# Performance work log

Hardware: AMD Instinct MI355X
Metric: run time of the kernel (lower is better)

The kernel has to match this reference:

```python
import jax, jax.numpy as jnp
import numpy as np

EPS = 1e-05


def layer_norm(x, a, b):
    m = jnp.mean(x, axis=-1, keepdims=True)
    v = jnp.var(x, axis=-1, keepdims=True)
    return a * (x - m) / jnp.sqrt(v + EPS) + b


def setup_inputs() -> dict:
    key = jax.random.key(0)
    ks = jax.random.split(key, 16)
    b, n, d, h = 1, 384, 128, 128
    s = 1.0 / np.sqrt(d)
    inp = {
        "x": jax.random.normal(ks[0], (b, n, n, d), dtype=jnp.float32),
        "norm_a": jnp.ones((d,), jnp.float32),
        "norm_b": jnp.zeros((d,), jnp.float32),
        "Wl": jax.random.normal(ks[1], (d, h), jnp.float32) * s,
        "bl": jnp.zeros((h,), jnp.float32),
        "Wr": jax.random.normal(ks[2], (d, h), jnp.float32) * s,
        "br": jnp.zeros((h,), jnp.float32),
        "Wlg": jax.random.normal(ks[3], (d, h), jnp.float32) * s,
        "blg": jnp.ones((h,), jnp.float32),
        "Wrg": jax.random.normal(ks[4], (d, h), jnp.float32) * s,
        "brg": jnp.ones((h,), jnp.float32),
        "Wog": jax.random.normal(ks[5], (d, h), jnp.float32) * s,
        "bog": jnp.ones((h,), jnp.float32),
        "on_a": jnp.ones((h,), jnp.float32),
        "on_b": jnp.zeros((h,), jnp.float32),
        "Wo": jax.random.normal(ks[6], (h, d), jnp.float32) * s,
        "bo": jnp.zeros((d,), jnp.float32),
    }
    return inp


def reference(x, norm_a, norm_b, Wl, bl, Wr, br, Wlg, blg, Wrg, brg, Wog, bog, on_a, on_b, Wo, bo):
    n = x.shape[1]
    xn = layer_norm(x, norm_a, norm_b)
    left = (xn @ Wl + bl) * jax.nn.sigmoid(xn @ Wlg + blg)
    right = (xn @ Wr + br) * jax.nn.sigmoid(xn @ Wrg + brg)
    out_gate = jax.nn.sigmoid(xn @ Wog + bog)
    # ingoing mix: out[b,i,j,d] = sum_k left[b,k,j,d] * right[b,k,i,d], in fp32
    out = jnp.einsum('bkjd,bkid->bijd', left.astype(jnp.float32), right.astype(jnp.float32)) / n
    out = out.astype(x.dtype)
    out = layer_norm(out, on_a, on_b) * out_gate
    return out @ Wo + bo
```

## Files before the change

### kernel.cpp

```cpp
#include <hip/hip_runtime.h>
#include <hip/hip_bf16.h>

#define NN 384
#define DD 128
#define MM (NN*NN)

typedef __attribute__((ext_vector_type(8))) short short8;
typedef __attribute__((ext_vector_type(4))) float f32x4;

__device__ __forceinline__ unsigned short f2bf(float f){
  unsigned u = __float_as_uint(f);
  u += 0x7fffu + ((u >> 16) & 1u);
  return (unsigned short)(u >> 16);
}
__device__ __forceinline__ float bf2f(unsigned short u){
  return __uint_as_float(((unsigned)u) << 16);
}
__device__ __forceinline__ float sigm(float x){
  return 1.0f / (1.0f + __expf(-x));
}
__device__ __forceinline__ unsigned cvtpk(float lo, float hi){
  unsigned r;
  asm("v_cvt_pk_bf16_f32 %0, %1, %2" : "=v"(r) : "v"(lo), "v"(hi));
  return r;
}
__device__ __forceinline__ f32x4 mfma16(short8 a, short8 b, f32x4 c){
  return __builtin_amdgcn_mfma_f32_16x16x32_bf16(a, b, c, 0, 0, 0);
}
__device__ __forceinline__ void gll16(const void* g, void* l){
  __builtin_amdgcn_global_load_lds(
      (const __attribute__((address_space(1))) unsigned int*)g,
      (__attribute__((address_space(3))) unsigned int*)l, 16, 0, 0);
}

__global__ void k_prep(const float* __restrict__ Wl, const float* __restrict__ Wlg,
                       const float* __restrict__ Wr, const float* __restrict__ Wrg,
                       const float* __restrict__ Wog, const float* __restrict__ Wo,
                       unsigned short* __restrict__ Wcat, unsigned short* __restrict__ Wot){
  int n = blockIdx.x;
  if(n < 640){
    const float* src; int col;
    if(n < 128){ src = Wl;  col = n; }
    else if(n < 256){ src = Wlg; col = n-128; }
    else if(n < 384){ src = Wr;  col = n-256; }
    else if(n < 512){ src = Wrg; col = n-384; }
    else            { src = Wog; col = n-512; }
    for(int k = threadIdx.x; k < 128; k += 64)
      Wcat[n*128 + k] = f2bf(src[k*128 + col]);
  } else {
    int c = n - 640;
    for(int k = threadIdx.x; k < 128; k += 64)
      Wot[c*128 + k] = f2bf(Wo[k*128 + c]);
  }
}

__global__ __launch_bounds__(256) void k_ln_x(const float* __restrict__ x,
    const float* __restrict__ na, const float* __restrict__ nb,
    unsigned short* __restrict__ xn){
  int wid = threadIdx.x >> 6, lane = threadIdx.x & 63;
  long r = (long)blockIdx.x*4 + wid;
  float2 v = *(const float2*)(x + r*DD + lane*2);
  float s  = v.x + v.y;
  float sq = v.x*v.x + v.y*v.y;
  #pragma unroll
  for(int m = 32; m >= 1; m >>= 1){ s += __shfl_xor(s, m); sq += __shfl_xor(sq, m); }
  float mean = s  * (1.0f/128.0f);
  float var  = sq * (1.0f/128.0f) - mean*mean;
  float rstd = rsqrtf(var + 1e-5f);
  float2 a = *(const float2*)(na + lane*2);
  float2 b = *(const float2*)(nb + lane*2);
  unsigned pk = (unsigned)f2bf(a.x*(v.x-mean)*rstd + b.x)
              | ((unsigned)f2bf(a.y*(v.y-mean)*rstd + b.y) << 16);
  *(unsigned*)(xn + r*DD + lane*2) = pk;
}

__global__ __launch_bounds__(256, 4) void k_proj(
    const unsigned short* __restrict__ xn, const unsigned short* __restrict__ Wcat,
    const float* __restrict__ bl, const float* __restrict__ blg,
    const float* __restrict__ br, const float* __restrict__ brg,
    unsigned short* __restrict__ Lt, unsigned short* __restrict__ Rt){
  __shared__ char lds[2][16384];
  const int tid = threadIdx.x;
  const int wid = tid >> 6, lane = tid & 63;
  const int lrow = lane & 15, lgrp = lane >> 4;
  const int b = blockIdx.x;
  const int f = b / 288;
  const int w = b % 288;

  const int ws = wid >> 1;
  const int wd = wid & 1;
  const int d  = f*32 + wd*16 + lrow;

  short8 bv[4], bg[4];
  #pragma unroll
  for(int ks = 0; ks < 4; ++ks){
    bv[ks] = *(const short8*)(Wcat + (ws*256 + d)*DD + ks*32 + lgrp*8);
    bg[ks] = *(const short8*)(Wcat + (ws*256 + 128 + d)*DD + ks*32 + lgrp*8);
  }
  const float b0v = (ws ? br  : bl )[d];
  const float b1v = (ws ? brg : blg)[d];
  const float sc  = ws ? 1.0f : (1.0f/384.0f);
  unsigned short* const base = (ws ? Rt : Lt) + (long)d*MM;

  auto stage = [&](int buf, int v){
    int j = v/6, kb = v%6;
    int rsub = lane >> 4, c = lane & 15;
    #pragma unroll
    for(int p = 0; p < 4; ++p){
      int r0 = p*16 + wid*4;
      int r = r0 + rsub;
      gll16(xn + ((long)(kb*64 + r)*NN + j)*DD + (c ^ (r & 7))*8, &lds[buf][r0*256]);
    }
  };

  stage(0, w*8);
  __syncthreads();
  int cur = 0;
  for(int i = 0; i < 8; ++i){
    int v = w*8 + i;
    if(i < 7) stage(cur^1, v+1);

    f32x4 zero = {0.f,0.f,0.f,0.f};
    f32x4 acc[4][2];
    #pragma unroll
    for(int a1=0;a1<4;++a1){ acc[a1][0] = zero; acc[a1][1] = zero; }

    #pragma unroll
    for(int ks = 0; ks < 4; ++ks){
      #pragma unroll
      for(int fr = 0; fr < 4; ++fr){
        int r = fr*16 + lrow;
        short8 af = *(const short8*)(&lds[cur][r*256 + (((ks*4+lgrp)*16) ^ ((r&7)<<4))]);
        acc[fr][0] = mfma16(af, bv[ks], acc[fr][0]);
        acc[fr][1] = mfma16(af, bg[ks], acc[fr][1]);
      }
    }

    int j = v/6, kb = v%6;
    unsigned short* dst = base + (long)j*NN + kb*64;
    #pragma unroll
    for(int fr = 0; fr < 4; ++fr){
      float v0 = (acc[fr][0][0] + b0v)*sigm(acc[fr][1][0] + b1v)*sc;
      float v1 = (acc[fr][0][1] + b0v)*sigm(acc[fr][1][1] + b1v)*sc;
      float v2 = (acc[fr][0][2] + b0v)*sigm(acc[fr][1][2] + b1v)*sc;
      float v3 = (acc[fr][0][3] + b0v)*sigm(acc[fr][1][3] + b1v)*sc;
      uint2 pk; pk.x = cvtpk(v0, v1); pk.y = cvtpk(v2, v3);
      *(uint2*)(dst + fr*16 + lgrp*4) = pk;
    }
    __syncthreads();
    cur ^= 1;
  }
}

__global__ __launch_bounds__(256) void k_einsum(
    const unsigned short* __restrict__ Rt, const unsigned short* __restrict__ Lt,
    unsigned short* __restrict__ mid){
  __shared__ char lds[65536];
  const int b = blockIdx.x;
  const int xcd = b & 7, slot = b >> 3;
  const int d = (slot/9)*8 + xcd;
  const int t = slot % 9;
  const int it = t/3, jt = t%3;
  const int i0 = it*128, j0 = jt*128;
  const unsigned short* Abase = Lt + (long)d*MM;
  const unsigned short* Bbase = Rt + (long)d*MM;
  const int wid = threadIdx.x >> 6, lane = threadIdx.x & 63;
  const int wr = wid >> 1, wc = wid & 1;
  const int lrow = lane & 15, lgrp = lane >> 4;

  auto stage = [&](int buf, int kt){
    int k = kt*64;
    int c = lane & 7;
    #pragma unroll
    for(int t8 = 0; t8 < 8; ++t8){
      int rr = wid*64 + t8*8 + (lane >> 3);
      int r = rr & 127;
      const unsigned short* src = (rr < 128) ? (Abase + (long)(j0+r)*NN + k)
                                             : (Bbase + (long)(i0+r)*NN + k);
      gll16(src + (c ^ (r & 7))*8, &lds[buf*32768 + (wid*64 + t8*8)*128]);
    }
  };

  f32x4 zero = {0.f,0.f,0.f,0.f};
  f32x4 acc[4][4];
  #pragma unroll
  for(int a1 = 0; a1 < 4; ++a1)
    #pragma unroll
    for(int a2 = 0; a2 < 4; ++a2) acc[a1][a2] = zero;

  stage(0, 0);
  __syncthreads();
  for(int kt = 0; kt < 6; ++kt){
    int cur = kt & 1;
    if(kt < 5) stage(cur ^ 1, kt + 1);
    const int base = cur*32768;
    #pragma unroll
    for(int ks = 0; ks < 2; ++ks){
      short8 af[4], bf[4];
      #pragma unroll
      for(int f = 0; f < 4; ++f){
        int rj = wr*64 + f*16 + lrow;
        af[f] = *(const short8*)(&lds[base + rj*128 + (((ks*4+lgrp)*16) ^ ((rj & 7) << 4))]);
        int ri = wc*64 + f*16 + lrow;
        bf[f] = *(const short8*)(&lds[base + 16384 + ri*128 + (((ks*4+lgrp)*16) ^ ((ri & 7) << 4))]);
      }
      #pragma unroll
      for(int fj = 0; fj < 4; ++fj)
        #pragma unroll
        for(int fi = 0; fi < 4; ++fi)
          acc[fj][fi] = mfma16(af[fj], bf[fi], acc[fj][fi]);
    }
    __syncthreads();
  }

  #pragma unroll
  for(int fj = 0; fj < 4; ++fj){
    int j = j0 + wr*64 + fj*16 + lgrp*4;
    #pragma unroll
    for(int fi = 0; fi < 4; ++fi){
      int i = i0 + wc*64 + fi*16 + lrow;
      uint2 pk;
      pk.x = cvtpk(acc[fj][fi][0], acc[fj][fi][1]);
      pk.y = cvtpk(acc[fj][fi][2], acc[fj][fi][3]);
      *(uint2*)(mid + (long)d*MM + (long)i*NN + j) = pk;
    }
  }
}

__global__ __launch_bounds__(256, 3) void k_final(
    const unsigned short* __restrict__ mid, const unsigned short* __restrict__ xn,
    const unsigned short* __restrict__ Wcat,
    const float* __restrict__ bog,
    const float* __restrict__ ona, const float* __restrict__ onb,
    const unsigned short* __restrict__ Wot, const float* __restrict__ bo,
    float* __restrict__ out){
  __shared__ char Xb[2][16384];
  __shared__ unsigned short midt[64][136];
  __shared__ float clds[512];
  const int tid = threadIdx.x;
  const int wid = tid >> 6, lane = tid & 63;
  const int lrow = lane & 15, lgrp = lane >> 4;
  const int jp = tid & 15, dr = tid >> 4;
  const int u0 = blockIdx.x * 3;

  uint2 mA[8], mB[8];

#define STAGE_XN(buf, uu) {                                                   \
    int i_ = (uu)/6, jj_ = ((uu)%6)*64;                                       \
    int rsub = lane >> 4, cc = lane & 15;                                     \
    _Pragma("unroll")                                                         \
    for(int p = 0; p < 4; ++p){                                               \
      int r0 = p*16 + wid*4;                                                  \
      int r = r0 + rsub;                                                      \
      gll16(xn + ((long)i_*NN + jj_ + r)*DD + (cc ^ (r & 7))*8,               \
            &Xb[buf][r0*256]);                                                \
    } }

#define LOAD_MID(reg, uu) {                                                   \
    int i_ = (uu)/6, jj_ = ((uu)%6)*64;                                       \
    const unsigned short* mp = mid + (long)i_*NN + jj_ + jp*4;                \
    _Pragma("unroll")                                                         \
    for(int p = 0; p < 8; ++p)                                                \
      reg[p] = *(const uint2*)(mp + (long)(p*16 + dr)*MM);                    \
  }

#define WRITE_MIDT(reg) {                                                     \
    _Pragma("unroll")                                                         \
    for(int p = 0; p < 8; ++p){                                               \
      int dd = p*16 + dr;                                                     \
      midt[jp*4+0][dd] = (unsigned short)(reg[p].x & 0xffffu);                \
      midt[jp*4+1][dd] = (unsigned short)(reg[p].x >> 16);                    \
      midt[jp*4+2][dd] = (unsigned short)(reg[p].y & 0xffffu);                \
      midt[jp*4+3][dd] = (unsigned short)(reg[p].y >> 16);                    \
    } }

  short8 ag[2][4], aw[2][4];
  #pragma unroll
  for(int cf = 0; cf < 2; ++cf)
    #pragma unroll
    for(int ks = 0; ks < 4; ++ks){
      ag[cf][ks] = *(const short8*)(Wcat + (512 + wid*32 + cf*16 + lrow)*DD + ks*32 + lgrp*8);
      aw[cf][ks] = *(const short8*)(Wot  + (      wid*32 + cf*16 + lrow)*DD + ks*32 + lgrp*8);
    }
  if(tid < 128){
    clds[tid]       = ona[tid];
    clds[128 + tid] = onb[tid];
    clds[256 + tid] = bog[tid];
    clds[384 + tid] = bo[tid];
  }

  STAGE_XN(0, u0);
  LOAD_MID(mA, u0);
  __syncthreads();

#define UNIT(T, MREG, MNXT, CUR) {                                            \
    const int u_ = u0 + (T);                                                  \
    const int iU = u_/6, jU = (u_%6)*64;                                      \
    if((T) < 2){ STAGE_XN((CUR)^1, u_+1); LOAD_MID(MNXT, u_+1); }             \
    WRITE_MIDT(MREG);                                                         \
    f32x4 zero_ = {0.f,0.f,0.f,0.f};                                          \
    f32x4 accg[2][4];                                                         \
    _Pragma("unroll")                                                         \
    for(int a1=0;a1<2;++a1){ _Pragma("unroll")                                \
      for(int a2=0;a2<4;++a2) accg[a1][a2] = zero_; }                         \
    _Pragma("unroll")                                                         \
    for(int ks = 0; ks < 4; ++ks){                                            \
      short8 bx[4];                                                           \
      _Pragma("unroll")                                                       \
      for(int mf = 0; mf < 4; ++mf){                                          \
        int r = mf*16 + lrow;                                                 \
        bx[mf] = *(const short8*)(&Xb[CUR][r*256 + (((ks*4+lgrp)*16) ^ ((r&7)<<4))]); \
      }                                                                       \
      _Pragma("unroll")                                                       \
      for(int cf = 0; cf < 2; ++cf){ _Pragma("unroll")                        \
        for(int mf = 0; mf < 4; ++mf)                                         \
          accg[cf][mf] = mfma16(ag[cf][ks], bx[mf], accg[cf][mf]); }          \
    }                                                                         \
    __syncthreads();   \
    _Pragma("unroll")                                                         \
    for(int cf = 0; cf < 2; ++cf){                                            \
      int c0 = wid*32 + cf*16 + lgrp*4;                                       \
      float4 g4 = *(const float4*)&clds[256 + c0];                            \
      _Pragma("unroll")                                                       \
      for(int mf = 0; mf < 4; ++mf){                                          \
        int rr = mf*16 + lrow;                                                \
        uint2 pk;                                                             \
        pk.x = cvtpk(sigm(accg[cf][mf][0]+g4.x), sigm(accg[cf][mf][1]+g4.y)); \
        pk.y = cvtpk(sigm(accg[cf][mf][2]+g4.z), sigm(accg[cf][mf][3]+g4.w)); \
        *(uint2*)(&Xb[CUR][rr*256 + ((c0*2) ^ ((rr&7)<<4))]) = pk;            \
      }                                                                       \
    }                                                                         \
    __syncthreads();                                      \
    {                                                                         \
      int j_ = tid >> 2, s_ = tid & 3;                                        \
      float sum = 0.f, sq = 0.f;                                              \
      _Pragma("unroll")                                                       \
      for(int o8 = 0; o8 < 4; ++o8){                                          \
        short8 h = *(const short8*)(&midt[j_][s_*32 + o8*8]);                 \
        _Pragma("unroll")                                                     \
        for(int q = 0; q < 8; ++q){                                           \
          float vq = bf2f((unsigned short)h[q]);                              \
          sum += vq; sq += vq*vq;                                             \
        }                                                                     \
      }                                                                       \
      sum += __shfl_xor(sum,1); sq += __shfl_xor(sq,1);                       \
      sum += __shfl_xor(sum,2); sq += __shfl_xor(sq,2);                       \
      float mean = sum*(1.f/128.f);                                           \
      float var  = sq *(1.f/128.f) - mean*mean;                               \
      float rstd = rsqrtf(var + 1e-5f);                                       \
      _Pragma("unroll")                                                       \
      for(int o = 0; o < 32; o += 4){                                         \
        int dd = s_*32 + o;                                                   \
        char* gp = &Xb[CUR][j_*256 + ((dd*2) ^ ((j_&7)<<4))];                 \
        uint2 gv = *(uint2*)gp;                                               \
        uint2 mv = *(const uint2*)(&midt[j_][dd]);                            \
        float m0 = bf2f((unsigned short)(mv.x & 0xffffu));                    \
        float m1 = bf2f((unsigned short)(mv.x >> 16));                        \
        float m2 = bf2f((unsigned short)(mv.y & 0xffffu));                    \
        float m3 = bf2f((unsigned short)(mv.y >> 16));                        \
        float4 a4 = *(const float4*)&clds[dd];                                \
        float4 b4 = *(const float4*)&clds[128 + dd];                          \
        float v0 = (a4.x*(m0-mean)*rstd + b4.x)*bf2f((unsigned short)(gv.x & 0xffffu)); \
        float v1 = (a4.y*(m1-mean)*rstd + b4.y)*bf2f((unsigned short)(gv.x >> 16));     \
        float v2 = (a4.z*(m2-mean)*rstd + b4.z)*bf2f((unsigned short)(gv.y & 0xffffu)); \
        float v3 = (a4.w*(m3-mean)*rstd + b4.w)*bf2f((unsigned short)(gv.y >> 16));     \
        uint2 pk; pk.x = cvtpk(v0, v1); pk.y = cvtpk(v2, v3);                 \
        *(uint2*)gp = pk;                                                     \
      }                                                                       \
    }                                                                         \
    __syncthreads();                                       \
    {                                                                         \
      f32x4 acco[2][4];                                                       \
      _Pragma("unroll")                                                       \
      for(int a1=0;a1<2;++a1){ _Pragma("unroll")                              \
        for(int a2=0;a2<4;++a2) acco[a1][a2] = zero_; }                       \
      _Pragma("unroll")                                                       \
      for(int ks = 0; ks < 4; ++ks){                                          \
        short8 bx[4];                                                         \
        _Pragma("unroll")                                                     \
        for(int mf = 0; mf < 4; ++mf){                                        \
          int r = mf*16 + lrow;                                               \
          bx[mf] = *(const short8*)(&Xb[CUR][r*256 + (((ks*4+lgrp)*16) ^ ((r&7)<<4))]); \
        }                                                                     \
        _Pragma("unroll")                                                     \
        for(int cf = 0; cf < 2; ++cf){ _Pragma("unroll")                      \
          for(int mf = 0; mf < 4; ++mf)                                       \
            acco[cf][mf] = mfma16(aw[cf][ks], bx[mf], acco[cf][mf]); }        \
      }                                                                       \
      _Pragma("unroll")                                                       \
      for(int cf = 0; cf < 2; ++cf){                                          \
        int c0 = wid*32 + cf*16 + lgrp*4;                                     \
        float4 b4 = *(const float4*)&clds[384 + c0];                          \
        _Pragma("unroll")                                                     \
        for(int mf = 0; mf < 4; ++mf){                                        \
          int jl = mf*16 + lrow;                                              \
          float4 v;                                                           \
          v.x = acco[cf][mf][0] + b4.x;                                       \
          v.y = acco[cf][mf][1] + b4.y;                                       \
          v.z = acco[cf][mf][2] + b4.z;                                       \
          v.w = acco[cf][mf][3] + b4.w;                                       \
          *(float4*)(out + ((long)iU*NN + jU + jl)*DD + c0) = v;              \
        }                                                                     \
      }                                                                       \
    }                                                                         \
    __syncthreads();  \
  }

  UNIT(0, mA, mB, 0)
  UNIT(1, mB, mA, 1)
  UNIT(2, mA, mB, 0)

#undef UNIT
#undef STAGE_XN
#undef LOAD_MID
#undef WRITE_MIDT
}

extern "C" void kernel_launch(void* const* d_in, const int* in_sizes, int n_in,
                              void* d_out, int out_size, void* d_ws, size_t ws_size,
                              hipStream_t stream){
  const float* x   = (const float*)d_in[0];
  const float* na  = (const float*)d_in[1];
  const float* nb  = (const float*)d_in[2];
  const float* Wl  = (const float*)d_in[3];
  const float* bl  = (const float*)d_in[4];
  const float* Wr  = (const float*)d_in[5];
  const float* br  = (const float*)d_in[6];
  const float* Wlg = (const float*)d_in[7];
  const float* blg = (const float*)d_in[8];
  const float* Wrg = (const float*)d_in[9];
  const float* brg = (const float*)d_in[10];
  const float* Wog = (const float*)d_in[11];
  const float* bog = (const float*)d_in[12];
  const float* ona = (const float*)d_in[13];
  const float* onb = (const float*)d_in[14];
  const float* Wo  = (const float*)d_in[15];
  const float* bo  = (const float*)d_in[16];
  float* out = (float*)d_out;

  char* ws = (char*)d_ws;
  const size_t SZ = (size_t)MM*DD*2;
  unsigned short* xn   = (unsigned short*)(ws);
  unsigned short* Lt   = (unsigned short*)(ws + SZ);
  unsigned short* Rt   = (unsigned short*)(ws + 2*SZ);
  unsigned short* mid  = (unsigned short*)(ws + 3*SZ);
  unsigned short* Wcat = (unsigned short*)(ws + 4*SZ);
  unsigned short* Wot  = (unsigned short*)(ws + 4*SZ + (size_t)640*128*2);

  k_prep  <<<768, 64, 0, stream>>>(Wl, Wlg, Wr, Wrg, Wog, Wo, Wcat, Wot);
  k_ln_x  <<<MM/4, 256, 0, stream>>>(x, na, nb, xn);
  k_proj  <<<1152, 256, 0, stream>>>(xn, Wcat, bl, blg, br, brg, Lt, Rt);
  k_einsum<<<1152, 256, 0, stream>>>(Rt, Lt, mid);
  k_final <<<768, 256, 0, stream>>>(mid, xn, Wcat, bog, ona, onb, Wot, bo, out);
}
```

Before: 166.7 us.

## Restructure final kernel: drop midt transpose, register LN stats, swap Wo MFMA roles

Reworks k_final so each thread loads mid with a d-contiguous mapping and keeps it in registers. This removes the midt LDS transpose buffer, and the output layer-norm statistics are reduced with shuffles plus a small LDS partial array. Gate and output biases are folded into the accumulator initialisation, and weights are reloaded per k-step instead of held in registers. The Wo projection swaps operand roles, so each wave owns 16 rows across all 128 output columns. Each block handles 2 units instead of 3, with occupancy 4 and 1152 blocks. The trade is scalar (non-vectorised) output stores and repeated global weight loads, in exchange for less LDS, fewer registers and fewer barriers.

New measurement: 237.0 us. 42.2% more time.

```diff
diff --git a/kernel.cpp b/kernel.cpp
--- a/kernel.cpp
+++ b/kernel.cpp
@@ -31,6 +31,10 @@
   __builtin_amdgcn_global_load_lds(
       (const __attribute__((address_space(1))) unsigned int*)g,
       (__attribute__((address_space(3))) unsigned int*)l, 16, 0, 0);
+}
+__device__ __forceinline__ void barL(){
+  asm volatile("s_waitcnt lgkmcnt(0)" ::: "memory");
+  __builtin_amdgcn_s_barrier();
 }
 
 __global__ void k_prep(const float* __restrict__ Wl, const float* __restrict__ Wlg,
@@ -227,7 +231,7 @@
   }
 }
 
-__global__ __launch_bounds__(256, 3) void k_final(
+__global__ __launch_bounds__(256, 4) void k_final(
     const unsigned short* __restrict__ mid, const unsigned short* __restrict__ xn,
     const unsigned short* __restrict__ Wcat,
     const float* __restrict__ bog,
@@ -235,76 +239,62 @@
     const unsigned short* __restrict__ Wot, const float* __restrict__ bo,
     float* __restrict__ out){
   __shared__ char Xb[2][16384];
-  __shared__ unsigned short midt[64][136];
+  __shared__ float4 wavep[128];
+  __shared__ float2 statB[64];
   __shared__ float clds[512];
   const int tid = threadIdx.x;
   const int wid = tid >> 6, lane = tid & 63;
   const int lrow = lane & 15, lgrp = lane >> 4;
   const int jp = tid & 15, dr = tid >> 4;
-  const int u0 = blockIdx.x * 3;
+  const int u0 = blockIdx.x * 2;
 
   uint2 mA[8], mB[8];
 
-#define STAGE_XN(buf, uu) {                                                   \
+#define LDMID(reg, uu) {                                                      \
+    int i_ = (uu)/6; long mbase = (long)i_*NN + ((uu)%6)*64 + jp*4;           \
+    _Pragma("unroll")                                                         \
+    for(int p = 0; p < 8; ++p)                                                \
+      reg[p] = *(const uint2*)(mid + (long)(dr*8 + p)*MM + mbase);            \
+  }
+
+#define STAGEXN(buf, uu) {                                                    \
     int i_ = (uu)/6, jj_ = ((uu)%6)*64;                                       \
     int rsub = lane >> 4, cc = lane & 15;                                     \
     _Pragma("unroll")                                                         \
     for(int p = 0; p < 4; ++p){                                               \
-      int r0 = p*16 + wid*4;                                                  \
-      int r = r0 + rsub;                                                      \
+      int r0 = p*16 + wid*4; int r = r0 + rsub;                               \
       gll16(xn + ((long)i_*NN + jj_ + r)*DD + (cc ^ (r & 7))*8,               \
             &Xb[buf][r0*256]);                                                \
     } }
 
-#define LOAD_MID(reg, uu) {                                                   \
-    int i_ = (uu)/6, jj_ = ((uu)%6)*64;                                       \
-    const unsigned short* mp = mid + (long)i_*NN + jj_ + jp*4;                \
-    _Pragma("unroll")                                                         \
-    for(int p = 0; p < 8; ++p)                                                \
-      reg[p] = *(const uint2*)(mp + (long)(p*16 + dr)*MM);                    \
-  }
-
-#define WRITE_MIDT(reg) {                                                     \
-    _Pragma("unroll")                                                         \
-    for(int p = 0; p < 8; ++p){                                               \
-      int dd = p*16 + dr;                                                     \
-      midt[jp*4+0][dd] = (unsigned short)(reg[p].x & 0xffffu);                \
-      midt[jp*4+1][dd] = (unsigned short)(reg[p].x >> 16);                    \
-      midt[jp*4+2][dd] = (unsigned short)(reg[p].y & 0xffffu);                \
-      midt[jp*4+3][dd] = (unsigned short)(reg[p].y >> 16);                    \
-    } }
-
-  short8 ag[2][4], aw[2][4];
-  #pragma unroll
-  for(int cf = 0; cf < 2; ++cf)
-    #pragma unroll
-    for(int ks = 0; ks < 4; ++ks){
-      ag[cf][ks] = *(const short8*)(Wcat + (512 + wid*32 + cf*16 + lrow)*DD + ks*32 + lgrp*8);
-      aw[cf][ks] = *(const short8*)(Wot  + (      wid*32 + cf*16 + lrow)*DD + ks*32 + lgrp*8);
-    }
+  STAGEXN(0, u0)
+  LDMID(mA, u0)
   if(tid < 128){
     clds[tid]       = ona[tid];
     clds[128 + tid] = onb[tid];
     clds[256 + tid] = bog[tid];
     clds[384 + tid] = bo[tid];
   }
-
-  STAGE_XN(0, u0);
-  LOAD_MID(mA, u0);
   __syncthreads();
 
-#define UNIT(T, MREG, MNXT, CUR) {                                            \
+#define UNIT(T, MC, MN, CUR) {                                                \
     const int u_ = u0 + (T);                                                  \
     const int iU = u_/6, jU = (u_%6)*64;                                      \
-    if((T) < 2){ STAGE_XN((CUR)^1, u_+1); LOAD_MID(MNXT, u_+1); }             \
-    WRITE_MIDT(MREG);                                                         \
-    f32x4 zero_ = {0.f,0.f,0.f,0.f};                                          \
+    if((T) == 0){ STAGEXN((CUR)^1, u_+1) LDMID(MN, u_+1) }                    \
+        \
     f32x4 accg[2][4];                                                         \
     _Pragma("unroll")                                                         \
-    for(int a1=0;a1<2;++a1){ _Pragma("unroll")                                \
-      for(int a2=0;a2<4;++a2) accg[a1][a2] = zero_; }                         \
+    for(int cf = 0; cf < 2; ++cf){                                            \
+      int c0 = wid*32 + cf*16 + lgrp*4;                                       \
+      float4 b4 = *(const float4*)&clds[256 + c0];                            \
+      _Pragma("unroll")                                                       \
+      for(int mf = 0; mf < 4; ++mf)                                           \
+        accg[cf][mf] = (f32x4){b4.x, b4.y, b4.z, b4.w};                       \
+    }                                                                         \
     _Pragma("unroll")                                                         \
     for(int ks = 0; ks < 4; ++ks){                                            \
+      short8 ag0 = *(const short8*)(Wcat + (512 + wid*32 + lrow)*DD + ks*32 + lgrp*8);       \
+      short8 ag1 = *(const short8*)(Wcat + (512 + wid*32 + 16 + lrow)*DD + ks*32 + lgrp*8);  \
       short8 bx[4];                                                           \
       _Pragma("unroll")                                                       \
       for(int mf = 0; mf < 4; ++mf){                                          \
@@ -312,108 +302,131 @@
         bx[mf] = *(const short8*)(&Xb[CUR][r*256 + (((ks*4+lgrp)*16) ^ ((r&7)<<4))]); \
       }                                                                       \
       _Pragma("unroll")                                                       \
-      for(int cf = 0; cf < 2; ++cf){ _Pragma("unroll")                        \
-        for(int mf = 0; mf < 4; ++mf)                                         \
-          accg[cf][mf] = mfma16(ag[cf][ks], bx[mf], accg[cf][mf]); }          \
-    }                                                                         \
-    __syncthreads();   \
+      for(int mf = 0; mf < 4; ++mf){                                          \
+        accg[0][mf] = mfma16(ag0, bx[mf], accg[0][mf]);                       \
+        accg[1][mf] = mfma16(ag1, bx[mf], accg[1][mf]);                       \
+      }                                                                       \
+    }                                                                         \
+    {                                                                         \
+      float s0=0,s1=0,s2=0,s3=0, q0=0,q1=0,q2=0,q3=0;                         \
+      _Pragma("unroll")                                                       \
+      for(int p = 0; p < 8; ++p){                                             \
+        float v0 = bf2f((unsigned short)(MC[p].x & 0xffffu));                 \
+        float v1 = bf2f((unsigned short)(MC[p].x >> 16));                     \
+        float v2 = bf2f((unsigned short)(MC[p].y & 0xffffu));                 \
+        float v3 = bf2f((unsigned short)(MC[p].y >> 16));                     \
+        s0 += v0; q0 += v0*v0;  s1 += v1; q1 += v1*v1;                        \
+        s2 += v2; q2 += v2*v2;  s3 += v3; q3 += v3*v3;                        \
+      }                                                                       \
+      _Pragma("unroll")                                                       \
+      for(int m = 16; m <= 32; m <<= 1){                                      \
+        s0 += __shfl_xor(s0,m); q0 += __shfl_xor(q0,m);                       \
+        s1 += __shfl_xor(s1,m); q1 += __shfl_xor(q1,m);                       \
+        s2 += __shfl_xor(s2,m); q2 += __shfl_xor(q2,m);                       \
+        s3 += __shfl_xor(s3,m); q3 += __shfl_xor(q3,m);                       \
+      }                                                                       \
+      if(lane < 16){                                                          \
+        wavep[(wid*16 + lane)*2 + 0] = (float4){s0, q0, s1, q1};              \
+        wavep[(wid*16 + lane)*2 + 1] = (float4){s2, q2, s3, q3};              \
+      }                                                                       \
+    }                                                                         \
+    barL();                                                           \
+                     \
     _Pragma("unroll")                                                         \
     for(int cf = 0; cf < 2; ++cf){                                            \
       int c0 = wid*32 + cf*16 + lgrp*4;                                       \
-      float4 g4 = *(const float4*)&clds[256 + c0];                            \
       _Pragma("unroll")                                                       \
       for(int mf = 0; mf < 4; ++mf){                                          \
-        int rr = mf*16 + lrow;                                                \
+        int j = mf*16 + lrow;                                                 \
         uint2 pk;                                                             \
-        pk.x = cvtpk(sigm(accg[cf][mf][0]+g4.x), sigm(accg[cf][mf][1]+g4.y)); \
-        pk.y = cvtpk(sigm(accg[cf][mf][2]+g4.z), sigm(accg[cf][mf][3]+g4.w)); \
-        *(uint2*)(&Xb[CUR][rr*256 + ((c0*2) ^ ((rr&7)<<4))]) = pk;            \
-      }                                                                       \
-    }                                                                         \
-    __syncthreads();                                      \
+        pk.x = cvtpk(sigm(accg[cf][mf][0]), sigm(accg[cf][mf][1]));           \
+        pk.y = cvtpk(sigm(accg[cf][mf][2]), sigm(accg[cf][mf][3]));           \
+        *(uint2*)(&Xb[CUR][j*256 + ((c0*2) ^ ((j&7)<<4))]) = pk;              \
+      }                                                                       \
+    }                                                                         \
+    if(tid < 64){                                                             \
+      int jpp = tid >> 2, jjj = tid & 3;                                      \
+      float s = 0.f, q = 0.f;                                                 \
+      _Pragma("unroll")                                                       \
+      for(int w = 0; w < 4; ++w){                                             \
+        float4 f = wavep[(w*16 + jpp)*2 + (jjj >> 1)];                        \
+        if(jjj & 1){ s += f.z; q += f.w; } else { s += f.x; q += f.y; }       \
+      }                                                                       \
+      float mean = s*(1.f/128.f);                                             \
+      float var  = q*(1.f/128.f) - mean*mean;                                 \
+      statB[tid] = (float2){mean, rsqrtf(var + 1e-5f)};                       \
+    }                                                                         \
+    barL();                                                           \
+                             \
     {                                                                         \
-      int j_ = tid >> 2, s_ = tid & 3;                                        \
-      float sum = 0.f, sq = 0.f;                                              \
-      _Pragma("unroll")                                                       \
-      for(int o8 = 0; o8 < 4; ++o8){                                          \
-        short8 h = *(const short8*)(&midt[j_][s_*32 + o8*8]);                 \
+      float4 a0 = *(const float4*)&clds[dr*8];                                \
+      float4 a1 = *(const float4*)&clds[dr*8 + 4];                            \
+      float4 b0 = *(const float4*)&clds[128 + dr*8];                          \
+      float4 b1 = *(const float4*)&clds[128 + dr*8 + 4];                      \
+      float av[8] = {a0.x,a0.y,a0.z,a0.w,a1.x,a1.y,a1.z,a1.w};                \
+      float bv[8] = {b0.x,b0.y,b0.z,b0.w,b1.x,b1.y,b1.z,b1.w};                \
+      _Pragma("unroll")                                                       \
+      for(int jj = 0; jj < 4; ++jj){                                          \
+        int j = jp*4 + jj;                                                    \
+        float2 mr = statB[j];                                                 \
+        char* gp = &Xb[CUR][j*256 + ((dr*16) ^ ((j&7)<<4))];                  \
+        short8 g8 = *(const short8*)gp;                                       \
+        float vv[8];                                                          \
         _Pragma("unroll")                                                     \
-        for(int q = 0; q < 8; ++q){                                           \
-          float vq = bf2f((unsigned short)h[q]);                              \
-          sum += vq; sq += vq*vq;                                             \
+        for(int p = 0; p < 8; ++p){                                           \
+          unsigned w = (jj & 1) ? ((jj & 2) ? (MC[p].y >> 16) : (MC[p].x >> 16))              \
+                                : ((jj & 2) ? (MC[p].y & 0xffffu) : (MC[p].x & 0xffffu));     \
+          float m = bf2f((unsigned short)w);                                  \
+          float g = bf2f((unsigned short)g8[p]);                              \
+          vv[p] = (av[p]*(m - mr.x)*mr.y + bv[p]) * g;                        \
         }                                                                     \
-      }                                                                       \
-      sum += __shfl_xor(sum,1); sq += __shfl_xor(sq,1);                       \
-      sum += __shfl_xor(sum,2); sq += __shfl_xor(sq,2);                       \
-      float mean = sum*(1.f/128.f);                                           \
-      float var  = sq *(1.f/128.f) - mean*mean;                               \
-      float rstd = rsqrtf(var + 1e-5f);                                       \
-      _Pragma("unroll")                                                       \
-      for(int o = 0; o < 32; o += 4){                                         \
-        int dd = s_*32 + o;                                                   \
-        char* gp = &Xb[CUR][j_*256 + ((dd*2) ^ ((j_&7)<<4))];                 \
-        uint2 gv = *(uint2*)gp;                                               \
-        uint2 mv = *(const uint2*)(&midt[j_][dd]);                            \
-        float m0 = bf2f((unsigned short)(mv.x & 0xffffu));                    \
-        float m1 = bf2f((unsigned short)(mv.x >> 16));                        \
-        float m2 = bf2f((unsigned short)(mv.y & 0xffffu));                    \
-        float m3 = bf2f((unsigned short)(mv.y >> 16));                        \
-        float4 a4 = *(const float4*)&clds[dd];                                \
-        float4 b4 = *(const float4*)&clds[128 + dd];                          \
-        float v0 = (a4.x*(m0-mean)*rstd + b4.x)*bf2f((unsigned short)(gv.x & 0xffffu)); \
-        float v1 = (a4.y*(m1-mean)*rstd + b4.y)*bf2f((unsigned short)(gv.x >> 16));     \
-        float v2 = (a4.z*(m2-mean)*rstd + b4.z)*bf2f((unsigned short)(gv.y & 0xffffu)); \
-        float v3 = (a4.w*(m3-mean)*rstd + b4.w)*bf2f((unsigned short)(gv.y >> 16));     \
-        uint2 pk; pk.x = cvtpk(v0, v1); pk.y = cvtpk(v2, v3);                 \
-        *(uint2*)gp = pk;                                                     \
-      }                                                                       \
-    }                                                                         \
-    __syncthreads();                                       \
+        short8 o;                                                             \
+        _Pragma("unroll")                                                     \
+        for(int p = 0; p < 4; ++p){                                           \
+          unsigned pk = cvtpk(vv[p*2], vv[p*2+1]);                            \
+          o[p*2] = (short)(pk & 0xffffu); o[p*2+1] = (short)(pk >> 16);       \
+        }                                                                     \
+        *(short8*)gp = o;                                                     \
+      }                                                                       \
+    }                                                                         \
+    barL();                                                           \
+          \
     {                                                                         \
-      f32x4 acco[2][4];                                                       \
-      _Pragma("unroll")                                                       \
-      for(int a1=0;a1<2;++a1){ _Pragma("unroll")                              \
-        for(int a2=0;a2<4;++a2) acco[a1][a2] = zero_; }                       \
+      f32x4 acc[8];                                                           \
+      _Pragma("unroll")                                                       \
+      for(int fc = 0; fc < 8; ++fc){                                          \
+        float bb = clds[384 + fc*16 + lrow];                                  \
+        acc[fc] = (f32x4){bb, bb, bb, bb};                                    \
+      }                                                                       \
       _Pragma("unroll")                                                       \
       for(int ks = 0; ks < 4; ++ks){                                          \
-        short8 bx[4];                                                         \
+        int r = wid*16 + lrow;                                                \
+        short8 af = *(const short8*)(&Xb[CUR][r*256 + (((ks*4+lgrp)*16) ^ ((r&7)<<4))]); \
         _Pragma("unroll")                                                     \
-        for(int mf = 0; mf < 4; ++mf){                                        \
-          int r = mf*16 + lrow;                                               \
-          bx[mf] = *(const short8*)(&Xb[CUR][r*256 + (((ks*4+lgrp)*16) ^ ((r&7)<<4))]); \
+        for(int fc = 0; fc < 8; ++fc){                                        \
+          short8 bw = *(const short8*)(Wot + (fc*16 + lrow)*DD + ks*32 + lgrp*8);        \
+          acc[fc] = mfma16(af, bw, acc[fc]);                                  \
         }                                                                     \
+      }                                                                       \
+      _Pragma("unroll")                                                       \
+      for(int fc = 0; fc < 8; ++fc){                                          \
+        int c = fc*16 + lrow;                                                 \
         _Pragma("unroll")                                                     \
-        for(int cf = 0; cf < 2; ++cf){ _Pragma("unroll")                      \
-          for(int mf = 0; mf < 4; ++mf)                                       \
-            acco[cf][mf] = mfma16(aw[cf][ks], bx[mf], acco[cf][mf]); }        \
-      }                                                                       \
-      _Pragma("unroll")                                                       \
-      for(int cf = 0; cf < 2; ++cf){                                          \
-        int c0 = wid*32 + cf*16 + lgrp*4;                                     \
-        float4 b4 = *(const float4*)&clds[384 + c0];                          \
-        _Pragma("unroll")                                                     \
-        for(int mf = 0; mf < 4; ++mf){                                        \
-          int jl = mf*16 + lrow;                                              \
-          float4 v;                                                           \
-          v.x = acco[cf][mf][0] + b4.x;                                       \
-          v.y = acco[cf][mf][1] + b4.y;                                       \
-          v.z = acco[cf][mf][2] + b4.z;                                       \
-          v.w = acco[cf][mf][3] + b4.w;                                       \
-          *(float4*)(out + ((long)iU*NN + jU + jl)*DD + c0) = v;              \
+        for(int q = 0; q < 4; ++q){                                           \
+          int jl = wid*16 + lgrp*4 + q;                                       \
+          out[((long)iU*NN + jU + jl)*DD + c] = acc[fc][q];                   \
         }                                                                     \
       }                                                                       \
     }                                                                         \
-    __syncthreads();  \
   }
 
   UNIT(0, mA, mB, 0)
+  __syncthreads();
   UNIT(1, mB, mA, 1)
-  UNIT(2, mA, mB, 0)
 
 #undef UNIT
-#undef STAGE_XN
-#undef LOAD_MID
-#undef WRITE_MIDT
+#undef STAGEXN
+#undef LDMID
 }
 
 extern "C" void kernel_launch(void* const* d_in, const int* in_sizes, int n_in,
@@ -451,5 +464,5 @@
   k_ln_x  <<<MM/4, 256, 0, stream>>>(x, na, nb, xn);
   k_proj  <<<1152, 256, 0, stream>>>(xn, Wcat, bl, blg, br, brg, Lt, Rt);
   k_einsum<<<1152, 256, 0, stream>>>(Rt, Lt, mid);
-  k_final <<<768, 256, 0, stream>>>(mid, xn, Wcat, bog, ona, onb, Wot, bo, out);
-}
+  k_final <<<1152, 256, 0, stream>>>(mid, xn, Wcat, bog, ona, onb, Wot, bo, out);
+}
```
